# Kernel tuning notes

Hardware: AMD Instinct MI355X
Metric: run time of the kernel (lower is better)

## Reference

```python
import jax, jax.numpy as jnp
import numpy as np

S = 1024   # speakers_per_batch
U = 64     # utterances_per_speaker
E = 256    # model_embedding_size


def setup_inputs() -> dict:
    key = jax.random.key(0)
    k1, _ = jax.random.split(key)
    # embeds as produced by forward(): relu'd then L2-normalized rows
    raw = jax.nn.relu(jax.random.normal(k1, (S * U, E), dtype=jnp.float32))
    embeds = raw / (jnp.linalg.norm(raw, axis=1, keepdims=True) + 1e-12)
    return {
        "embeds": embeds,
        "similarity_weight": jnp.array([10.0], dtype=jnp.float32),
        "similarity_bias": jnp.array([-5.0], dtype=jnp.float32),
    }


def reference(embeds, similarity_weight, similarity_bias):
    e = embeds.reshape(S, U, E)                      # [S,U,E]
    # inclusive centroids (per speaker)
    c_incl = jnp.mean(e, axis=1)                     # [S,E]
    incl_norm = jnp.linalg.norm(c_incl, axis=1)      # [S]
    # exclusive centroids (leave-one-out per utterance)
    c_excl = (jnp.sum(e, axis=1, keepdims=True) - e) / (U - 1)  # [S,U,E]
    excl_norm = jnp.linalg.norm(c_excl, axis=2)      # [S,U]
    # off-diagonal (k != j): cosine vs inclusive centroid of speaker k
    sim = jnp.einsum('jue,ke->juk', e, c_incl) / incl_norm       # [S,U,S]
    # diagonal (k == j): cosine vs own exclusive centroid
    diag = jnp.einsum('jue,jue->ju', e, c_excl) / excl_norm      # [S,U]
    idx = jnp.arange(S)
    sim = sim.at[idx, :, idx].set(diag)
    sim = sim * similarity_weight[0] + similarity_bias[0]
    # cross-entropy against ground truth speaker ids
    logits = sim.reshape(S * U, S)                   # [SU,S]
    gt = jnp.repeat(jnp.arange(S), U)                # [SU]
    logp = jax.nn.log_softmax(logits, axis=-1)
    loss = -jnp.mean(jnp.take_along_axis(logp, gt[:, None], axis=1))
    preds = jnp.argmax(logits, axis=1)
    accuracy = jnp.mean((preds == gt).astype(jnp.float32))
    return loss, accuracy
```

## Files before the change

### kernel.cpp

```cpp
#include <hip/hip_runtime.h>
#include <math.h>

#define NS 1024
#define NU 64
#define NE 256

typedef __attribute__((ext_vector_type(8))) short short8;
typedef __attribute__((ext_vector_type(4))) float f32x4;
typedef __attribute__((ext_vector_type(4))) unsigned short us4;

__device__ static inline unsigned short f2bf(float f) {
  unsigned int u = __float_as_uint(f);
  unsigned int r = (u + 0x7fffu + ((u >> 16) & 1u)) >> 16;
  return (unsigned short)r;
}


__global__ __launch_bounds__(256) void centroid_kernel(
    const float* __restrict__ embeds, unsigned short* __restrict__ Cb,
    float* __restrict__ normsum, float* __restrict__ ssumG,
    unsigned int* __restrict__ packG, float* __restrict__ out) {
  int k = blockIdx.x;
  int t = threadIdx.x;
  if (t < 64) {
    ssumG[k * 64 + t] = 0.f;
    packG[k * 64 + t] = 0u;
  }
  int wave = t >> 6, e4 = t & 63;
  const float4* base =
      (const float4*)(embeds + (size_t)k * NU * NE) + wave * 16 * 64 + e4;
  float4 s = {0.f, 0.f, 0.f, 0.f};
#pragma unroll
  for (int i = 0; i < 16; ++i) {
    float4 v = base[i * 64];
    s.x += v.x; s.y += v.y; s.z += v.z; s.w += v.w;
  }
  __shared__ float4 ps[4][64];
  ps[wave][e4] = s;
  __syncthreads();
  if (t < 64) {
    float4 a = ps[0][t], b = ps[1][t], c = ps[2][t], d = ps[3][t];
    float4 s4;
    s4.x = a.x + b.x + c.x + d.x;
    s4.y = a.y + b.y + c.y + d.y;
    s4.z = a.z + b.z + c.z + d.z;
    s4.w = a.w + b.w + c.w + d.w;
    float sq = s4.x * s4.x + s4.y * s4.y + s4.z * s4.z + s4.w * s4.w;
#pragma unroll
    for (int off = 32; off; off >>= 1) sq += __shfl_xor(sq, off, 64);
    float nrm = sqrtf(sq);
    float inv = 1.f / nrm;
    int G = (k >> 4) * 8 + (t >> 3);
    int off = (((t >> 1) & 3) * 16 + (k & 15)) * 8 + (t & 1) * 4;
    us4 v;
    v[0] = f2bf(s4.x * inv);
    v[1] = f2bf(s4.y * inv);
    v[2] = f2bf(s4.z * inv);
    v[3] = f2bf(s4.w * inv);
    *(us4*)(Cb + (size_t)G * 512 + off) = v;
    if (t == 0) {
      normsum[k] = nrm;
      if (k == 0) { out[0] = 0.f; out[1] = 0.f; }
    }
  }
}

__global__ __launch_bounds__(256, 2) void main_kernel(
    const float* __restrict__ embeds, const unsigned short* __restrict__ Cb,
    const float* __restrict__ normsum, const float* __restrict__ wp,
    const float* __restrict__ bp, float* __restrict__ ssumG,
    unsigned int* __restrict__ packG, float* __restrict__ gtlG) {
  int t = threadIdx.x;
  int wave = t >> 6, lane = t & 63;
  int c = lane & 15, q = lane >> 4;
  int b = blockIdx.x;
  int rg = b >> 1;
  int h = b & 1;
  int jspk = rg * 2 + (wave >> 1);
  int r0 = rg * 128 + wave * 32;

  float w = *wp, bia = *bp;
  const float L2E = 1.4426950408889634f;
  float M0 = fabsf(w) + bia;
  float wl = w * L2E;
  float cl = (bia - M0) * L2E;
  float ns = normsum[jspk];

  const short8* cb8 = (const short8*)Cb;
  int fb = h * 32 * 512 + lane;

  short8 bfA[4], bfB[4];
#pragma unroll
  for (int s = 0; s < 4; ++s) bfA[s] = cb8[fb + s * 64];
#pragma unroll
  for (int s = 0; s < 4; ++s) bfB[s] = cb8[fb + (4 + s) * 64];

  short8 af[2][8];
  float n2p[2];
#pragma unroll
  for (int mt = 0; mt < 2; ++mt) {
    const float* rowp = embeds + (size_t)(r0 + mt * 16 + c) * NE;
    float acc2 = 0.f;
#pragma unroll
    for (int s = 0; s < 8; ++s) {
      int k0 = s * 32 + q * 8;
      float4 x = *(const float4*)(rowp + k0);
      float4 y = *(const float4*)(rowp + k0 + 4);
      acc2 += x.x * x.x + x.y * x.y + x.z * x.z + x.w * x.w;
      acc2 += y.x * y.x + y.y * y.y + y.z * y.z + y.w * y.w;
      short8 f;
      f[0] = (short)f2bf(x.x); f[1] = (short)f2bf(x.y);
      f[2] = (short)f2bf(x.z); f[3] = (short)f2bf(x.w);
      f[4] = (short)f2bf(y.x); f[5] = (short)f2bf(y.y);
      f[6] = (short)f2bf(y.z); f[7] = (short)f2bf(y.w);
      af[mt][s] = f;
    }
    n2p[mt] = acc2;
  }
#pragma unroll
  for (int mt = 0; mt < 2; ++mt) {
    n2p[mt] += __shfl_xor(n2p[mt], 16, 64);
    n2p[mt] += __shfl_xor(n2p[mt], 32, 64);
  }
  float n2d[2][4];
#pragma unroll
  for (int mt = 0; mt < 2; ++mt)
#pragma unroll
    for (int r = 0; r < 4; ++r)
      n2d[mt][r] = __shfl(n2p[mt], q * 4 + r, 64);

  float ssum[2][4];
  unsigned int pm[2][4];
#pragma unroll
  for (int mt = 0; mt < 2; ++mt)
#pragma unroll
    for (int r = 0; r < 4; ++r) {
      ssum[mt][r] = 0.f;
      pm[mt][r] = 0u;
    }

#pragma unroll 1
  for (int T = 0; T < 32; ++T) {
    f32x4 acc0 = {0.f, 0.f, 0.f, 0.f};
    f32x4 acc1 = {0.f, 0.f, 0.f, 0.f};
    int nb = fb + (T + 1) * 512;
    bool more = (T + 1 < 32);
#pragma unroll
    for (int s = 0; s < 4; ++s) {
      acc0 = __builtin_amdgcn_mfma_f32_16x16x32_bf16(af[0][s], bfA[s], acc0,
                                                     0, 0, 0);
      acc1 = __builtin_amdgcn_mfma_f32_16x16x32_bf16(af[1][s], bfA[s], acc1,
                                                     0, 0, 0);
    }
    if (more) {
#pragma unroll
      for (int s = 0; s < 4; ++s) bfA[s] = cb8[nb + s * 64];
    }
#pragma unroll
    for (int s = 0; s < 4; ++s) {
      acc0 = __builtin_amdgcn_mfma_f32_16x16x32_bf16(af[0][4 + s], bfB[s],
                                                     acc0, 0, 0, 0);
      acc1 = __builtin_amdgcn_mfma_f32_16x16x32_bf16(af[1][4 + s], bfB[s],
                                                     acc1, 0, 0, 0);
    }
    if (more) {
#pragma unroll
      for (int s = 0; s < 4; ++s) bfB[s] = cb8[nb + (4 + s) * 64];
    }

    int gt = h * 32 + T;
    int col = gt * 16 + c;
    bool diagstep = ((jspk >> 4) == gt);
#pragma unroll
    for (int mt = 0; mt < 2; ++mt) {
      f32x4 a = mt ? acc1 : acc0;
      if (diagstep && c == (jspk & 15)) {
#pragma unroll
        for (int r = 0; r < 4; ++r) {
          float d = a[r];
          float n2 = n2d[mt][r];
          float Sv = d * ns;
          float den = fmaxf(fmaf(ns, ns, n2) - 2.f * Sv, 1e-30f);
          float val = (Sv - n2) * __frsqrt_rn(den);
          gtlG[r0 + mt * 16 + q * 4 + r] = fmaf(w, val, bia);
          a[r] = val;
        }
      }
#pragma unroll
      for (int r = 0; r < 4; ++r) {
        float p = exp2f(fmaf(a[r], wl, cl));
        ssum[mt][r] += p;
        unsigned int pk =
            (__float_as_uint(p) & 0xfffffc00u) | (unsigned)(1023 - col);
        pm[mt][r] = pm[mt][r] > pk ? pm[mt][r] : pk;
      }
    }
  }

#pragma unroll
  for (int mt = 0; mt < 2; ++mt)
#pragma unroll
    for (int r = 0; r < 4; ++r) {
      float s = ssum[mt][r];
      s += __shfl_xor(s, 1, 64);
      s += __shfl_xor(s, 2, 64);
      s += __shfl_xor(s, 4, 64);
      s += __shfl_xor(s, 8, 64);
      unsigned int m = pm[mt][r];
#pragma unroll
      for (int off = 1; off < 16; off <<= 1) {
        unsigned int m2 = __shfl_xor((int)m, off, 64);
        m = m > m2 ? m : m2;
      }
      if (c == 0) {
        int row = r0 + mt * 16 + q * 4 + r;
        atomicAdd(&ssumG[row], s);
        atomicMax(&packG[row], m);
      }
    }
}

__global__ __launch_bounds__(256) void reduce_kernel(
    const float* __restrict__ ssumG, const unsigned int* __restrict__ packG,
    const float* __restrict__ gtlG, const float* __restrict__ wp,
    const float* __restrict__ bp, float* __restrict__ out) {
  int i = blockIdx.x * 256 + threadIdx.x;
  int spk = i >> 6;
  float w = *wp, bia = *bp;
  float M0 = fabsf(w) + bia;
  float lossr = M0 + __logf(ssumG[i]) - gtlG[i];
  int amax = 1023 - (int)(packG[i] & 1023u);
  float corr = (amax == spk) ? 1.f : 0.f;
#pragma unroll
  for (int off = 32; off; off >>= 1) {
    lossr += __shfl_xor(lossr, off, 64);
    corr += __shfl_xor(corr, off, 64);
  }
  __shared__ float pl[4], pc[4];
  int wave = threadIdx.x >> 6, lane = threadIdx.x & 63;
  if (lane == 0) { pl[wave] = lossr; pc[wave] = corr; }
  __syncthreads();
  if (threadIdx.x == 0) {
    const float inv = 1.f / (float)(NS * NU);
    atomicAdd(&out[0], (pl[0] + pl[1] + pl[2] + pl[3]) * inv);
    atomicAdd(&out[1], (pc[0] + pc[1] + pc[2] + pc[3]) * inv);
  }
}

extern "C" void kernel_launch(void* const* d_in, const int* in_sizes, int n_in,
                              void* d_out, int out_size, void* d_ws,
                              size_t ws_size, hipStream_t stream) {
  const float* embeds = (const float*)d_in[0];
  const float* w = (const float*)d_in[1];
  const float* b = (const float*)d_in[2];
  float* out = (float*)d_out;
  char* ws = (char*)d_ws;
  unsigned short* Cb = (unsigned short*)ws;
  unsigned int* packG = (unsigned int*)(ws + (512 << 10));
  float* ssumG = (float*)(ws + (768 << 10));
  float* gtlG = (float*)(ws + (1024 << 10));
  float* normsum = (float*)(ws + (1280 << 10));

  centroid_kernel<<<NS, 256, 0, stream>>>(embeds, Cb, normsum, ssumG, packG,
                                          out);
  main_kernel<<<1024, 256, 0, stream>>>(embeds, Cb, normsum, w, b, ssumG,
                                        packG, gtlG);
  reduce_kernel<<<NS * NU / 256, 256, 0, stream>>>(ssumG, packG, gtlG, w, b,
                                                   out);
}
```

Before: 165.1 us.

## Switch similarity GEMM to FP8 MFMA and double rows per wave

Embeddings and normalized centroids are now quantized to FP8 (packed via cvt_pk_fp8) and multiplied with the 16x16x32 fp8 MFMA instead of bf16. Each wave now handles 64 rows (four M-tiles) instead of 32, halving the grid to 512 blocks so each loaded centroid fragment is reused across more rows. This halves centroid bytes and raises MFMA throughput, but FP8 precision may perturb logits, argmax accuracy and the diagonal term. It also raises register pressure under the 2-blocks-per-SIMD launch bound.

```diff
diff --git a/kernel.cpp b/kernel.cpp
--- a/kernel.cpp
+++ b/kernel.cpp
@@ -5,19 +5,19 @@
 #define NU 64
 #define NE 256
 
-typedef __attribute__((ext_vector_type(8))) short short8;
 typedef __attribute__((ext_vector_type(4))) float f32x4;
-typedef __attribute__((ext_vector_type(4))) unsigned short us4;
-
-__device__ static inline unsigned short f2bf(float f) {
-  unsigned int u = __float_as_uint(f);
-  unsigned int r = (u + 0x7fffu + ((u >> 16) & 1u)) >> 16;
-  return (unsigned short)r;
+
+__device__ static inline unsigned int pk4_fp8(float a, float b, float c,
+                                              float d) {
+  int r = 0;
+  r = __builtin_amdgcn_cvt_pk_fp8_f32(a, b, r, false);
+  r = __builtin_amdgcn_cvt_pk_fp8_f32(c, d, r, true);
+  return (unsigned int)r;
 }
 
 
 __global__ __launch_bounds__(256) void centroid_kernel(
-    const float* __restrict__ embeds, unsigned short* __restrict__ Cb,
+    const float* __restrict__ embeds, unsigned int* __restrict__ Cb,
     float* __restrict__ normsum, float* __restrict__ ssumG,
     unsigned int* __restrict__ packG, float* __restrict__ out) {
   int k = blockIdx.x;
@@ -50,14 +50,10 @@
     for (int off = 32; off; off >>= 1) sq += __shfl_xor(sq, off, 64);
     float nrm = sqrtf(sq);
     float inv = 1.f / nrm;
-    int G = (k >> 4) * 8 + (t >> 3);
-    int off = (((t >> 1) & 3) * 16 + (k & 15)) * 8 + (t & 1) * 4;
-    us4 v;
-    v[0] = f2bf(s4.x * inv);
-    v[1] = f2bf(s4.y * inv);
-    v[2] = f2bf(s4.z * inv);
-    v[3] = f2bf(s4.w * inv);
-    *(us4*)(Cb + (size_t)G * 512 + off) = v;
+    unsigned int v = pk4_fp8(s4.x * inv, s4.y * inv, s4.z * inv, s4.w * inv);
+    int idx = (k >> 4) * 1024 + (t >> 3) * 128 +
+              ((((t >> 1) & 3) * 16 + (k & 15)) << 1) + (t & 1);
+    Cb[idx] = v;
     if (t == 0) {
       normsum[k] = nrm;
       if (k == 0) { out[0] = 0.f; out[1] = 0.f; }
@@ -66,7 +62,7 @@
 }
 
 __global__ __launch_bounds__(256, 2) void main_kernel(
-    const float* __restrict__ embeds, const unsigned short* __restrict__ Cb,
+    const float* __restrict__ embeds, const long* __restrict__ Cb,
     const float* __restrict__ normsum, const float* __restrict__ wp,
     const float* __restrict__ bp, float* __restrict__ ssumG,
     unsigned int* __restrict__ packG, float* __restrict__ gtlG) {
@@ -76,8 +72,8 @@
   int b = blockIdx.x;
   int rg = b >> 1;
   int h = b & 1;
-  int jspk = rg * 2 + (wave >> 1);
-  int r0 = rg * 128 + wave * 32;
+  int r0 = rg * 256 + wave * 64;
+  int jspk = r0 >> 6;
 
   float w = *wp, bia = *bp;
   const float L2E = 1.4426950408889634f;
@@ -86,19 +82,18 @@
   float cl = (bia - M0) * L2E;
   float ns = normsum[jspk];
 
-  const short8* cb8 = (const short8*)Cb;
   int fb = h * 32 * 512 + lane;
 
-  short8 bfA[4], bfB[4];
-#pragma unroll
-  for (int s = 0; s < 4; ++s) bfA[s] = cb8[fb + s * 64];
-#pragma unroll
-  for (int s = 0; s < 4; ++s) bfB[s] = cb8[fb + (4 + s) * 64];
-
-  short8 af[2][8];
-  float n2p[2];
-#pragma unroll
-  for (int mt = 0; mt < 2; ++mt) {
+  long bfA[4], bfB[4];
+#pragma unroll
+  for (int s = 0; s < 4; ++s) bfA[s] = Cb[fb + s * 64];
+#pragma unroll
+  for (int s = 0; s < 4; ++s) bfB[s] = Cb[fb + (4 + s) * 64];
+
+  long af[4][8];
+  float n2p[4];
+#pragma unroll
+  for (int mt = 0; mt < 4; ++mt) {
     const float* rowp = embeds + (size_t)(r0 + mt * 16 + c) * NE;
     float acc2 = 0.f;
 #pragma unroll
@@ -108,31 +103,28 @@
       float4 y = *(const float4*)(rowp + k0 + 4);
       acc2 += x.x * x.x + x.y * x.y + x.z * x.z + x.w * x.w;
       acc2 += y.x * y.x + y.y * y.y + y.z * y.z + y.w * y.w;
-      short8 f;
-      f[0] = (short)f2bf(x.x); f[1] = (short)f2bf(x.y);
-      f[2] = (short)f2bf(x.z); f[3] = (short)f2bf(x.w);
-      f[4] = (short)f2bf(y.x); f[5] = (short)f2bf(y.y);
-      f[6] = (short)f2bf(y.z); f[7] = (short)f2bf(y.w);
-      af[mt][s] = f;
+      unsigned int lo = pk4_fp8(x.x, x.y, x.z, x.w);
+      unsigned int hi = pk4_fp8(y.x, y.y, y.z, y.w);
+      af[mt][s] = (long)(((unsigned long long)hi << 32) | lo);
     }
     n2p[mt] = acc2;
   }
 #pragma unroll
-  for (int mt = 0; mt < 2; ++mt) {
+  for (int mt = 0; mt < 4; ++mt) {
     n2p[mt] += __shfl_xor(n2p[mt], 16, 64);
     n2p[mt] += __shfl_xor(n2p[mt], 32, 64);
   }
-  float n2d[2][4];
-#pragma unroll
-  for (int mt = 0; mt < 2; ++mt)
+  float n2d[4][4];
+#pragma unroll
+  for (int mt = 0; mt < 4; ++mt)
 #pragma unroll
     for (int r = 0; r < 4; ++r)
       n2d[mt][r] = __shfl(n2p[mt], q * 4 + r, 64);
 
-  float ssum[2][4];
-  unsigned int pm[2][4];
-#pragma unroll
-  for (int mt = 0; mt < 2; ++mt)
+  float ssum[4][4];
+  unsigned int pm[4][4];
+#pragma unroll
+  for (int mt = 0; mt < 4; ++mt)
 #pragma unroll
     for (int r = 0; r < 4; ++r) {
       ssum[mt][r] = 0.f;
@@ -141,39 +133,38 @@
 
 #pragma unroll 1
   for (int T = 0; T < 32; ++T) {
-    f32x4 acc0 = {0.f, 0.f, 0.f, 0.f};
-    f32x4 acc1 = {0.f, 0.f, 0.f, 0.f};
+    f32x4 acc[4];
+#pragma unroll
+    for (int mt = 0; mt < 4; ++mt) acc[mt] = (f32x4){0.f, 0.f, 0.f, 0.f};
     int nb = fb + (T + 1) * 512;
     bool more = (T + 1 < 32);
 #pragma unroll
-    for (int s = 0; s < 4; ++s) {
-      acc0 = __builtin_amdgcn_mfma_f32_16x16x32_bf16(af[0][s], bfA[s], acc0,
-                                                     0, 0, 0);
-      acc1 = __builtin_amdgcn_mfma_f32_16x16x32_bf16(af[1][s], bfA[s], acc1,
-                                                     0, 0, 0);
-    }
+    for (int s = 0; s < 4; ++s)
+#pragma unroll
+      for (int mt = 0; mt < 4; ++mt)
+        acc[mt] = __builtin_amdgcn_mfma_f32_16x16x32_fp8_fp8(
+            af[mt][s], bfA[s], acc[mt], 0, 0, 0);
     if (more) {
 #pragma unroll
-      for (int s = 0; s < 4; ++s) bfA[s] = cb8[nb + s * 64];
-    }
-#pragma unroll
-    for (int s = 0; s < 4; ++s) {
-      acc0 = __builtin_amdgcn_mfma_f32_16x16x32_bf16(af[0][4 + s], bfB[s],
-                                                     acc0, 0, 0, 0);
-      acc1 = __builtin_amdgcn_mfma_f32_16x16x32_bf16(af[1][4 + s], bfB[s],
-                                                     acc1, 0, 0, 0);
-    }
+      for (int s = 0; s < 4; ++s) bfA[s] = Cb[nb + s * 64];
+    }
+#pragma unroll
+    for (int s = 0; s < 4; ++s)
+#pragma unroll
+      for (int mt = 0; mt < 4; ++mt)
+        acc[mt] = __builtin_amdgcn_mfma_f32_16x16x32_fp8_fp8(
+            af[mt][4 + s], bfB[s], acc[mt], 0, 0, 0);
     if (more) {
 #pragma unroll
-      for (int s = 0; s < 4; ++s) bfB[s] = cb8[nb + (4 + s) * 64];
+      for (int s = 0; s < 4; ++s) bfB[s] = Cb[nb + (4 + s) * 64];
     }
 
     int gt = h * 32 + T;
     int col = gt * 16 + c;
     bool diagstep = ((jspk >> 4) == gt);
 #pragma unroll
-    for (int mt = 0; mt < 2; ++mt) {
-      f32x4 a = mt ? acc1 : acc0;
+    for (int mt = 0; mt < 4; ++mt) {
+      f32x4 a = acc[mt];
       if (diagstep && c == (jspk & 15)) {
 #pragma unroll
         for (int r = 0; r < 4; ++r) {
@@ -198,7 +189,7 @@
   }
 
 #pragma unroll
-  for (int mt = 0; mt < 2; ++mt)
+  for (int mt = 0; mt < 4; ++mt)
 #pragma unroll
     for (int r = 0; r < 4; ++r) {
       float s = ssum[mt][r];
@@ -255,16 +246,16 @@
   const float* b = (const float*)d_in[2];
   float* out = (float*)d_out;
   char* ws = (char*)d_ws;
-  unsigned short* Cb = (unsigned short*)ws;
-  unsigned int* packG = (unsigned int*)(ws + (512 << 10));
-  float* ssumG = (float*)(ws + (768 << 10));
-  float* gtlG = (float*)(ws + (1024 << 10));
-  float* normsum = (float*)(ws + (1280 << 10));
+  unsigned int* Cb = (unsigned int*)ws;
+  unsigned int* packG = (unsigned int*)(ws + (256 << 10));
+  float* ssumG = (float*)(ws + (512 << 10));
+  float* gtlG = (float*)(ws + (768 << 10));
+  float* normsum = (float*)(ws + (1024 << 10));
 
   centroid_kernel<<<NS, 256, 0, stream>>>(embeds, Cb, normsum, ssumG, packG,
                                           out);
-  main_kernel<<<1024, 256, 0, stream>>>(embeds, Cb, normsum, w, b, ssumG,
-                                        packG, gtlG);
+  main_kernel<<<512, 256, 0, stream>>>(embeds, (const long*)Cb, normsum, w, b,
+                                       ssumG, packG, gtlG);
   reduce_kernel<<<NS * NU / 256, 256, 0, stream>>>(ssumG, packG, gtlG, w, b,
                                                    out);
 }
```

New measurement: 159.3 us. 3.5% less time.
